# Kernel optimization log

Hardware: AMD Instinct MI355X
Metric: run time of the kernel (lower is better)

The kernel has to match this reference:

```python
import jax, jax.numpy as jnp
import numpy as np


def gcn_conv(x, src, dst, W, b, n_nodes):
    # PyG GCNConv with self-loops and symmetric normalization.
    h = x @ W                                        # [N, out]
    deg = jax.ops.segment_sum(jnp.ones_like(dst, dtype=h.dtype), dst,
                              num_segments=n_nodes)  # includes self-loops
    dinv = jnp.where(deg > 0, jax.lax.rsqrt(deg), 0.0)
    norm = dinv[src] * dinv[dst]                     # [E]
    msg = h[src] * norm[:, None]                     # gather + scale
    out = jax.ops.segment_sum(msg, dst, num_segments=n_nodes)
    return out + b


def setup_inputs() -> dict:
    key = jax.random.key(0)
    ks = jax.random.split(key, 16)
    N, E, F_IN, H, H2, C = 150000, 2400000, 61, 32, 16, 3
    x = jax.random.normal(ks[0], (N, F_IN), dtype=jnp.float32)
    edge_index = jax.random.randint(ks[1], (2, E), 0, N, dtype=jnp.int64)

    def lin(k, fin, fout):
        kw, kb = jax.random.split(k)
        s = 1.0 / np.sqrt(fin)
        W = jax.random.uniform(kw, (fin, fout), jnp.float32, -s, s)
        b = jax.random.uniform(kb, (fout,), jnp.float32, -s, s)
        return W, b

    W1, b1 = lin(ks[2], F_IN, H)
    W2, b2 = lin(ks[3], H, H)
    W3, b3 = lin(ks[4], H, H)
    W4, b4 = lin(ks[5], H, H)
    Wl1, bl1 = lin(ks[6], H, H2)
    Wl2, bl2 = lin(ks[7], H2, C)
    return {"x": x, "edge_index": edge_index,
            "W1": W1, "b1": b1, "W2": W2, "b2": b2,
            "W3": W3, "b3": b3, "W4": W4, "b4": b4,
            "Wl1": Wl1, "bl1": bl1, "Wl2": Wl2, "bl2": bl2}


def reference(x, edge_index, W1, b1, W2, b2, W3, b3, W4, b4, Wl1, bl1, Wl2, bl2):
    n = x.shape[0]
    loops = jnp.arange(n, dtype=edge_index.dtype)
    src = jnp.concatenate([edge_index[0], loops])
    dst = jnp.concatenate([edge_index[1], loops])
    # dropout p=0.25 is identity in eval mode
    h = jax.nn.relu(gcn_conv(x, src, dst, W1, b1, n))
    h = jax.nn.relu(gcn_conv(h, src, dst, W2, b2, n))
    h = jax.nn.relu(gcn_conv(h, src, dst, W3, b3, n))
    h = jax.nn.relu(gcn_conv(h, src, dst, W4, b4, n))
    g = jnp.sum(h, axis=0)                           # sum pool over all nodes -> [32]
    g = jax.nn.relu(g @ Wl1 + bl1)
    return g @ Wl2 + bl2                             # [3]
```

## Files before the change

### kernel.cpp

```cpp
#include <hip/hip_runtime.h>
#include <hip/hip_fp16.h>

#define F_IN 61
#define H 32
#define BUCK_BITS 8
#define BUCK_SZ   256
#define CHUNK     8192
#define XPAD 72

typedef _Float16 f16x8 __attribute__((ext_vector_type(8)));
typedef float    f32x4 __attribute__((ext_vector_type(4)));

__global__ __launch_bounds__(256) void scan1_kernel(const int* __restrict__ in,
                                                    int* __restrict__ scanned,
                                                    int* __restrict__ btot, int n) {
    __shared__ int s[256];
    int tid = threadIdx.x;
    int i = blockIdx.x * 256 + tid;
    int v = (i < n) ? in[i] : 0;
    s[tid] = v;
    __syncthreads();
    for (int off = 1; off < 256; off <<= 1) {
        int t = (tid >= off) ? s[tid - off] : 0;
        __syncthreads();
        s[tid] += t;
        __syncthreads();
    }
    if (i < n) scanned[i] = s[tid] - v;
    if (tid == 255) btot[blockIdx.x] = s[255];
}

__global__ __launch_bounds__(1024) void scan2_kernel(int* __restrict__ btot, int nB) {
    __shared__ int s[1024];
    int tid = threadIdx.x;
    int v = (tid < nB) ? btot[tid] : 0;
    s[tid] = v;
    __syncthreads();
    for (int off = 1; off < 1024; off <<= 1) {
        int t = (tid >= off) ? s[tid - off] : 0;
        __syncthreads();
        s[tid] += t;
        __syncthreads();
    }
    if (tid < nB) btot[tid] = s[tid] - v;
}

__global__ __launch_bounds__(256) void histA_kernel(const int* __restrict__ ei,
                                                    int* __restrict__ counts,
                                                    float* __restrict__ gs,
                                                    int E, int B, int nbuck) {
    __shared__ int h[640];
    int tid = threadIdx.x;
    if (blockIdx.x == 0) {
        #pragma unroll
        for (int r = 0; r < 8; r++) gs[r * 256 + tid] = 0.f;
    }
    for (int i = tid; i < nbuck; i += 256) h[i] = 0;
    __syncthreads();
    int e0 = blockIdx.x * CHUNK;
    int e1 = e0 + CHUNK; if (e1 > E) e1 = E;
    for (int e = e0 + tid; e < e1; e += 256)
        atomicAdd(&h[ei[E + e] >> BUCK_BITS], 1);
    __syncthreads();
    for (int i = tid; i < nbuck; i += 256) counts[i * B + blockIdx.x] = h[i];
}

__global__ __launch_bounds__(256) void binB_kernel(const int* __restrict__ ei,
                                                   const int* __restrict__ countsS,
                                                   const int* __restrict__ btot,
                                                   int* __restrict__ tmp,
                                                   int E, int B, int nbuck) {
    __shared__ int lcur[640];
    int tid = threadIdx.x;
    for (int i = tid; i < nbuck; i += 256) {
        int ci = i * B + blockIdx.x;
        lcur[i] = countsS[ci] + btot[ci >> 8];
    }
    __syncthreads();
    int e0 = blockIdx.x * CHUNK;
    int e1 = e0 + CHUNK; if (e1 > E) e1 = E;
    for (int e = e0 + tid; e < e1; e += 256) {
        int s = ei[e];
        int d = ei[E + e];
        int pos = atomicAdd(&lcur[d >> BUCK_BITS], 1);
        tmp[pos] = (s << BUCK_BITS) | (d & (BUCK_SZ - 1));
    }
}

__global__ __launch_bounds__(256) void binC_kernel(const int* __restrict__ countsS,
                                                   const int* __restrict__ btot,
                                                   const int* __restrict__ tmp,
                                                   int* __restrict__ src_sorted,
                                                   int* __restrict__ row_start,
                                                   float* __restrict__ dinv,
                                                   __half* __restrict__ bufA,
                                                   __half* __restrict__ bufB,
                                                   int N, int E, int B, int nbuck) {
    __shared__ int hist[BUCK_SZ];
    __shared__ int pre[BUCK_SZ];
    __shared__ int lcur[BUCK_SZ];
    int tid = threadIdx.x;
    int b = blockIdx.x;
    int base = b << BUCK_BITS;
    if (b == 0 && tid < H) {
        bufA[(size_t)N * H + tid] = __float2half(0.f);
        bufB[(size_t)N * H + tid] = __float2half(0.f);
    }
    int c0 = b * B;
    int e0 = countsS[c0] + btot[c0 >> 8];
    int e1 = E;
    if (b + 1 < nbuck) {
        int c1 = (b + 1) * B;
        e1 = countsS[c1] + btot[c1 >> 8];
    }
    hist[tid] = 0;
    __syncthreads();
    for (int e = e0 + tid; e < e1; e += 256)
        atomicAdd(&hist[tmp[e] & (BUCK_SZ - 1)], 1);
    __syncthreads();
    int v = hist[tid];
    pre[tid] = v;
    __syncthreads();
    for (int off = 1; off < 256; off <<= 1) {
        int t = (tid >= off) ? pre[tid - off] : 0;
        __syncthreads();
        pre[tid] += t;
        __syncthreads();
    }
    int excl = pre[tid] - v;
    int node = base + tid;
    if (node < N) {
        row_start[node] = e0 + excl;
        dinv[node] = rsqrtf((float)v + 1.0f);
        if (node == N - 1) row_start[N] = E;
    }
    lcur[tid] = e0 + excl;
    __syncthreads();
    for (int e = e0 + tid; e < e1; e += 256) {
        int p = tmp[e];
        int pos = atomicAdd(&lcur[p & (BUCK_SZ - 1)], 1);
        src_sorted[pos] = (p >> BUCK_BITS) << 6;
    }
}

__global__ __launch_bounds__(256) void gemm1_kernel(const float* __restrict__ x,
                                                    const float* __restrict__ W,
                                                    const float* __restrict__ dinv,
                                                    __half* __restrict__ h, int N) {
    __shared__ _Float16 Wt[H * XPAD];
    __shared__ _Float16 xs[64 * XPAD];
    int tid = threadIdx.x;
    for (int i = tid; i < 2048; i += 256) {
        int k = i >> 5, f = i & 31;
        Wt[f * XPAD + k] = (k < F_IN) ? (_Float16)W[k * H + f] : (_Float16)0.f;
    }
    int nb = blockIdx.x * 64;
    int navail = N - nb; if (navail > 64) navail = 64;
    int lim = navail * F_IN;
    const float* xb = x + (long long)nb * F_IN;
    for (int i = tid; i < 64 * F_IN; i += 256) {
        int n = i / F_IN, k = i - n * F_IN;
        xs[n * XPAD + k] = (i < lim) ? (_Float16)xb[i] : (_Float16)0.f;
    }
    if (tid < 192) {
        int n = tid / 3, k = F_IN + (tid - n * 3);
        xs[n * XPAD + k] = (_Float16)0.f;
    }
    __syncthreads();
    int w = tid >> 6, lane = tid & 63;
    int l16 = lane & 15, g = lane >> 4;
    const f16x8* ax  = (const f16x8*)&xs[(w * 16 + l16) * XPAD + g * 8];
    const f16x8* bw0 = (const f16x8*)&Wt[l16 * XPAD + g * 8];
    const f16x8* bw1 = (const f16x8*)&Wt[(16 + l16) * XPAD + g * 8];
    f16x8 a0 = ax[0],  a1 = ax[4];
    f16x8 b00 = bw0[0], b01 = bw0[4];
    f16x8 b10 = bw1[0], b11 = bw1[4];
    f32x4 acc0 = {0.f, 0.f, 0.f, 0.f};
    f32x4 acc1 = {0.f, 0.f, 0.f, 0.f};
    acc0 = __builtin_amdgcn_mfma_f32_16x16x32_f16(a0, b00, acc0, 0, 0, 0);
    acc0 = __builtin_amdgcn_mfma_f32_16x16x32_f16(a1, b01, acc0, 0, 0, 0);
    acc1 = __builtin_amdgcn_mfma_f32_16x16x32_f16(a0, b10, acc1, 0, 0, 0);
    acc1 = __builtin_amdgcn_mfma_f32_16x16x32_f16(a1, b11, acc1, 0, 0, 0);
    int nodebase = nb + w * 16 + g * 4;
    #pragma unroll
    for (int r = 0; r < 4; r++) {
        int node = nodebase + r;
        if (node < N) {
            float di = dinv[node];
            h[(long long)node * H + l16]      = __float2half(acc0[r] * di);
            h[(long long)node * H + 16 + l16] = __float2half(acc1[r] * di);
        }
    }
}

__global__ __launch_bounds__(256) void agg_gemm_kernel(const int* __restrict__ row_start,
                                                       const int* __restrict__ src_sorted,
                                                       const float* __restrict__ dinv,
                                                       const __half* __restrict__ hs,
                                                       const float* __restrict__ b,
                                                       const float* __restrict__ Wn,
                                                       __half* __restrict__ hout, int N) {
    __shared__ float Ws[H * H];
    __shared__ float t[8 * H];
    int tid = threadIdx.x;
    for (int i = tid; i < H * H; i += 256) Ws[i] = Wn[i];
    int nl = tid >> 5;
    int lane32 = tid & 31;
    int p = lane32 >> 4;
    int fp = lane32 & 15;
    int node = blockIdx.x * 8 + nl;
    int zoff = N << 6;
    __half2 accA = __floats2half2_rn(0.f, 0.f);
    __half2 accB = __floats2half2_rn(0.f, 0.f);
    if (node < N) {
        const char* hbase = (const char*)hs + (fp << 2);
        int e0 = row_start[node], e1 = row_start[node + 1];
        int idxv = (e0 + lane32 < e1) ? src_sorted[e0 + lane32] : zoff;
        for (int base = e0; base < e1; base += 32) {
            int w = e1 - base; if (w > 32) w = 32;
            int idxN = (base + 32 + lane32 < e1) ? src_sorted[base + 32 + lane32] : zoff;
            for (int j = 0; j < w; j += 16) {
                int offs[8];
                #pragma unroll
                for (int k = 0; k < 8; k++) offs[k] = __shfl(idxv, j + 2 * k + p, 32);
                unsigned g[8];
                #pragma unroll
                for (int k = 0; k < 8; k++) g[k] = *(const unsigned*)(hbase + offs[k]);
                #pragma unroll
                for (int k = 0; k < 8; k += 2) {
                    accA = __hadd2(accA, *(__half2*)&g[k]);
                    accB = __hadd2(accB, *(__half2*)&g[k + 1]);
                }
            }
            idxv = idxN;
        }
    }
    __half2 accH = __hadd2(accA, accB);
    float2 acc = __half22float2(accH);
    acc.x += __shfl_xor(acc.x, 16, 32);
    acc.y += __shfl_xor(acc.y, 16, 32);
    if (node < N && p == 0) {
        float di = dinv[node];
        unsigned sv = *(const unsigned*)((const char*)hs + ((long long)node << 6) + (fp << 2));
        float2 s2 = __half22float2(*(__half2*)&sv);
        float2 bv = ((const float2*)b)[fp];
        float rx = fmaxf(di * (acc.x + s2.x) + bv.x, 0.f);
        float ry = fmaxf(di * (acc.y + s2.y) + bv.y, 0.f);
        ((float2*)&t[nl * H])[fp] = make_float2(rx, ry);
    }
    __syncthreads();
    if (node < N) {
        int f = lane32;
        float s = 0.f;
        #pragma unroll
        for (int k = 0; k < H; k++) s += t[nl * H + k] * Ws[k * H + f];
        hout[(long long)node * H + f] = __float2half(s * dinv[node]);
    }
}

__global__ __launch_bounds__(256) void agg_pool_kernel(const int* __restrict__ row_start,
                                                       const int* __restrict__ src_sorted,
                                                       const float* __restrict__ dinv,
                                                       const __half* __restrict__ hs,
                                                       const float* __restrict__ b,
                                                       float* __restrict__ gs, int N) {
    __shared__ float t[8 * H];
    int tid = threadIdx.x;
    int nl = tid >> 5;
    int lane32 = tid & 31;
    int p = lane32 >> 4;
    int fp = lane32 & 15;
    int node = blockIdx.x * 8 + nl;
    int zoff = N << 6;
    __half2 accA = __floats2half2_rn(0.f, 0.f);
    __half2 accB = __floats2half2_rn(0.f, 0.f);
    if (node < N) {
        const char* hbase = (const char*)hs + (fp << 2);
        int e0 = row_start[node], e1 = row_start[node + 1];
        int idxv = (e0 + lane32 < e1) ? src_sorted[e0 + lane32] : zoff;
        for (int base = e0; base < e1; base += 32) {
            int w = e1 - base; if (w > 32) w = 32;
            int idxN = (base + 32 + lane32 < e1) ? src_sorted[base + 32 + lane32] : zoff;
            for (int j = 0; j < w; j += 16) {
                int offs[8];
                #pragma unroll
                for (int k = 0; k < 8; k++) offs[k] = __shfl(idxv, j + 2 * k + p, 32);
                unsigned g[8];
                #pragma unroll
                for (int k = 0; k < 8; k++) g[k] = *(const unsigned*)(hbase + offs[k]);
                #pragma unroll
                for (int k = 0; k < 8; k += 2) {
                    accA = __hadd2(accA, *(__half2*)&g[k]);
                    accB = __hadd2(accB, *(__half2*)&g[k + 1]);
                }
            }
            idxv = idxN;
        }
    }
    __half2 accH = __hadd2(accA, accB);
    float2 acc = __half22float2(accH);
    acc.x += __shfl_xor(acc.x, 16, 32);
    acc.y += __shfl_xor(acc.y, 16, 32);
    if (p == 0) {
        float2 r = make_float2(0.f, 0.f);
        if (node < N) {
            float di = dinv[node];
            unsigned sv = *(const unsigned*)((const char*)hs + ((long long)node << 6) + (fp << 2));
            float2 s2 = __half22float2(*(__half2*)&sv);
            float2 bv = ((const float2*)b)[fp];
            r.x = fmaxf(di * (acc.x + s2.x) + bv.x, 0.f);
            r.y = fmaxf(di * (acc.y + s2.y) + bv.y, 0.f);
        }
        ((float2*)&t[nl * H])[fp] = r;
    }
    __syncthreads();
    if (tid < H) {
        float s = 0.f;
        #pragma unroll
        for (int rI = 0; rI < 8; rI++) s += t[rI * H + tid];
        atomicAdd(&gs[(blockIdx.x & 63) * H + tid], s);
    }
}

__global__ __launch_bounds__(64) void head_kernel(const float* __restrict__ gs,
                                                  const float* __restrict__ Wl1,
                                                  const float* __restrict__ bl1,
                                                  const float* __restrict__ Wl2,
                                                  const float* __restrict__ bl2,
                                                  float* __restrict__ out) {
    __shared__ float gg[H];
    __shared__ float t[16];
    int tid = threadIdx.x;
    if (tid < H) {
        float s = 0.f;
        for (int c = 0; c < 64; c++) s += gs[c * H + tid];
        gg[tid] = s;
    }
    __syncthreads();
    if (tid < 16) {
        float s = bl1[tid];
        #pragma unroll
        for (int k = 0; k < 32; k++) s += gg[k] * Wl1[k * 16 + tid];
        t[tid] = fmaxf(s, 0.f);
    }
    __syncthreads();
    if (tid < 3) {
        float s = bl2[tid];
        #pragma unroll
        for (int k = 0; k < 16; k++) s += t[k] * Wl2[k * 3 + tid];
        out[tid] = s;
    }
}

extern "C" void kernel_launch(void* const* d_in, const int* in_sizes, int n_in,
                              void* d_out, int out_size, void* d_ws, size_t ws_size,
                              hipStream_t stream) {
    const float* x   = (const float*)d_in[0];
    const int*   ei  = (const int*)d_in[1];
    const float* W1  = (const float*)d_in[2];
    const float* b1  = (const float*)d_in[3];
    const float* W2  = (const float*)d_in[4];
    const float* b2  = (const float*)d_in[5];
    const float* W3  = (const float*)d_in[6];
    const float* b3  = (const float*)d_in[7];
    const float* W4  = (const float*)d_in[8];
    const float* b4  = (const float*)d_in[9];
    const float* Wl1 = (const float*)d_in[10];
    const float* bl1 = (const float*)d_in[11];
    const float* Wl2 = (const float*)d_in[12];
    const float* bl2 = (const float*)d_in[13];
    float* out = (float*)d_out;

    const int N = in_sizes[0] / F_IN;
    const int E = in_sizes[1] / 2;
    const int nbuck = (N + BUCK_SZ - 1) >> BUCK_BITS;
    const int B = (E + CHUNK - 1) / CHUNK;
    const int nC = nbuck * B;

    char* ws = (char*)d_ws;
    size_t off = 0;
    auto alloc = [&](size_t bytes) {
        char* p = ws + off;
        off += (bytes + 255) & ~(size_t)255;
        return p;
    };
    float* dinv       = (float*)alloc((size_t)N * 4);
    int*   row_start  = (int*)alloc((size_t)(N + 1) * 4);
    int*   counts     = (int*)alloc((size_t)nC * 4);
    int*   countsS    = (int*)alloc((size_t)nC * 4);
    int*   btot2      = (int*)alloc(((size_t)nC / 256 + 2) * 4);
    int*   src_sorted = (int*)alloc((size_t)E * 4);
    int*   tmp        = (int*)alloc((size_t)E * 4);
    __half* bufA      = (__half*)alloc((size_t)(N + 1) * H * 2);
    __half* bufB      = (__half*)alloc((size_t)(N + 1) * H * 2);
    float* gs         = (float*)alloc(64 * H * 4);

    const int TB = 256;
    const int gC  = (nC + TB - 1) / TB;
    const int gN8 = (N + 7) / 8;
    const int gN64 = (N + 63) / 64;

    histA_kernel<<<B, TB, 0, stream>>>(ei, counts, gs, E, B, nbuck);
    scan1_kernel<<<gC, TB, 0, stream>>>(counts, countsS, btot2, nC);
    scan2_kernel<<<1, 1024, 0, stream>>>(btot2, gC);
    binB_kernel<<<B, TB, 0, stream>>>(ei, countsS, btot2, tmp, E, B, nbuck);
    binC_kernel<<<nbuck, TB, 0, stream>>>(countsS, btot2, tmp, src_sorted, row_start,
                                          dinv, bufA, bufB, N, E, B, nbuck);

    gemm1_kernel<<<gN64, TB, 0, stream>>>(x, W1, dinv, bufA, N);
    agg_gemm_kernel<<<gN8, TB, 0, stream>>>(row_start, src_sorted, dinv, bufA, b1, W2, bufB, N);
    agg_gemm_kernel<<<gN8, TB, 0, stream>>>(row_start, src_sorted, dinv, bufB, b2, W3, bufA, N);
    agg_gemm_kernel<<<gN8, TB, 0, stream>>>(row_start, src_sorted, dinv, bufA, b3, W4, bufB, N);
    agg_pool_kernel<<<gN8, TB, 0, stream>>>(row_start, src_sorted, dinv, bufB, b4, gs, N);

    head_kernel<<<1, 64, 0, stream>>>(gs, Wl1, bl1, Wl2, bl2, out);
}
```

Baseline: 361.2 us.

## Stage bucket edges in LDS for binning and use nontemporal index loads and stores

The bin kernel now caches each bucket's edges in shared memory when they fit, and scatters the sorted sources into an LDS output buffer before writing them out coalesced. This avoids rereading tmp from global memory and avoids scattered global writes. Separately, the aggregation kernels read src_sorted with nontemporal loads and write hout with nontemporal stores, so the streaming index traffic leaves cache room for the gathered features. The 48KB of extra LDS per block may lower occupancy in binC, and the nontemporal hout store could hurt if the next layer rereads it from cache.

```diff
diff --git a/kernel.cpp b/kernel.cpp
--- a/kernel.cpp
+++ b/kernel.cpp
@@ -7,6 +7,7 @@
 #define BUCK_SZ   256
 #define CHUNK     8192
 #define XPAD 72
+#define CMAX 6144
 
 typedef _Float16 f16x8 __attribute__((ext_vector_type(8)));
 typedef float    f32x4 __attribute__((ext_vector_type(4)));
@@ -99,6 +100,8 @@
     __shared__ int hist[BUCK_SZ];
     __shared__ int pre[BUCK_SZ];
     __shared__ int lcur[BUCK_SZ];
+    __shared__ int ebuf[CMAX];
+    __shared__ int obuf[CMAX];
     int tid = threadIdx.x;
     int b = blockIdx.x;
     int base = b << BUCK_BITS;
@@ -113,10 +116,20 @@
         int c1 = (b + 1) * B;
         e1 = countsS[c1] + btot[c1 >> 8];
     }
+    int cnt = e1 - e0;
+    bool fits = (cnt <= CMAX);
     hist[tid] = 0;
     __syncthreads();
-    for (int e = e0 + tid; e < e1; e += 256)
-        atomicAdd(&hist[tmp[e] & (BUCK_SZ - 1)], 1);
+    if (fits) {
+        for (int j = tid; j < cnt; j += 256) {
+            int p = tmp[e0 + j];
+            ebuf[j] = p;
+            atomicAdd(&hist[p & (BUCK_SZ - 1)], 1);
+        }
+    } else {
+        for (int j = tid; j < cnt; j += 256)
+            atomicAdd(&hist[tmp[e0 + j] & (BUCK_SZ - 1)], 1);
+    }
     __syncthreads();
     int v = hist[tid];
     pre[tid] = v;
@@ -134,12 +147,23 @@
         dinv[node] = rsqrtf((float)v + 1.0f);
         if (node == N - 1) row_start[N] = E;
     }
-    lcur[tid] = e0 + excl;
-    __syncthreads();
-    for (int e = e0 + tid; e < e1; e += 256) {
-        int p = tmp[e];
-        int pos = atomicAdd(&lcur[p & (BUCK_SZ - 1)], 1);
-        src_sorted[pos] = (p >> BUCK_BITS) << 6;
+    lcur[tid] = fits ? excl : (e0 + excl);
+    __syncthreads();
+    if (fits) {
+        for (int j = tid; j < cnt; j += 256) {
+            int p = ebuf[j];
+            int pos = atomicAdd(&lcur[p & (BUCK_SZ - 1)], 1);
+            obuf[pos] = (p >> BUCK_BITS) << 6;
+        }
+        __syncthreads();
+        for (int j = tid; j < cnt; j += 256)
+            src_sorted[e0 + j] = obuf[j];
+    } else {
+        for (int j = tid; j < cnt; j += 256) {
+            int p = tmp[e0 + j];
+            int pos = atomicAdd(&lcur[p & (BUCK_SZ - 1)], 1);
+            src_sorted[pos] = (p >> BUCK_BITS) << 6;
+        }
     }
 }
 
@@ -215,10 +239,12 @@
     if (node < N) {
         const char* hbase = (const char*)hs + (fp << 2);
         int e0 = row_start[node], e1 = row_start[node + 1];
-        int idxv = (e0 + lane32 < e1) ? src_sorted[e0 + lane32] : zoff;
+        int idxv = zoff;
+        if (e0 + lane32 < e1) idxv = __builtin_nontemporal_load(src_sorted + e0 + lane32);
         for (int base = e0; base < e1; base += 32) {
             int w = e1 - base; if (w > 32) w = 32;
-            int idxN = (base + 32 + lane32 < e1) ? src_sorted[base + 32 + lane32] : zoff;
+            int idxN = zoff;
+            if (base + 32 + lane32 < e1) idxN = __builtin_nontemporal_load(src_sorted + base + 32 + lane32);
             for (int j = 0; j < w; j += 16) {
                 int offs[8];
                 #pragma unroll
@@ -254,7 +280,9 @@
         float s = 0.f;
         #pragma unroll
         for (int k = 0; k < H; k++) s += t[nl * H + k] * Ws[k * H + f];
-        hout[(long long)node * H + f] = __float2half(s * dinv[node]);
+        __half hv = __float2half(s * dinv[node]);
+        __builtin_nontemporal_store(__half_as_ushort(hv),
+                                    (unsigned short*)&hout[(long long)node * H + f]);
     }
 }
 
@@ -277,10 +305,12 @@
     if (node < N) {
         const char* hbase = (const char*)hs + (fp << 2);
         int e0 = row_start[node], e1 = row_start[node + 1];
-        int idxv = (e0 + lane32 < e1) ? src_sorted[e0 + lane32] : zoff;
+        int idxv = zoff;
+        if (e0 + lane32 < e1) idxv = __builtin_nontemporal_load(src_sorted + e0 + lane32);
         for (int base = e0; base < e1; base += 32) {
             int w = e1 - base; if (w > 32) w = 32;
-            int idxN = (base + 32 + lane32 < e1) ? src_sorted[base + 32 + lane32] : zoff;
+            int idxN = zoff;
+            if (base + 32 + lane32 < e1) idxN = __builtin_nontemporal_load(src_sorted + base + 32 + lane32);
             for (int j = 0; j < w; j += 16) {
                 int offs[8];
                 #pragma unroll
```

Result: no change. 363.5 us (+0.6%).

## Replace two-level bucketed CSR build with global-atomic degree count and scatter

Applied to the files above, without the earlier changes.

Replaces the bucketed counting sort (per-chunk bucket histograms, scan, binning into a temp array, per-bucket local sort) with a simpler CSR build: global atomic degree count per node, a scan over N nodes, then a scatter of edges into place using global atomic cursors. This drops the tmp array and one full pass over the edges, and the scan kernel now handles four elements per thread so it covers more than 1024 blocks. In exchange it relies on random global atomics on 150K counters, which may contend or be slower than LDS atomics, and the order of edges within each row is no longer deterministic.

```diff
diff --git a/kernel.cpp b/kernel.cpp
--- a/kernel.cpp
+++ b/kernel.cpp
@@ -3,9 +3,6 @@
 
 #define F_IN 61
 #define H 32
-#define BUCK_BITS 8
-#define BUCK_SZ   256
-#define CHUNK     8192
 #define XPAD 72
 
 typedef _Float16 f16x8 __attribute__((ext_vector_type(8)));
@@ -33,8 +30,13 @@
 __global__ __launch_bounds__(1024) void scan2_kernel(int* __restrict__ btot, int nB) {
     __shared__ int s[1024];
     int tid = threadIdx.x;
-    int v = (tid < nB) ? btot[tid] : 0;
-    s[tid] = v;
+    int base = tid << 2;
+    int v0 = (base + 0 < nB) ? btot[base + 0] : 0;
+    int v1 = (base + 1 < nB) ? btot[base + 1] : 0;
+    int v2 = (base + 2 < nB) ? btot[base + 2] : 0;
+    int v3 = (base + 3 < nB) ? btot[base + 3] : 0;
+    int sum = v0 + v1 + v2 + v3;
+    s[tid] = sum;
     __syncthreads();
     for (int off = 1; off < 1024; off <<= 1) {
         int t = (tid >= off) ? s[tid - off] : 0;
@@ -42,104 +44,59 @@
         s[tid] += t;
         __syncthreads();
     }
-    if (tid < nB) btot[tid] = s[tid] - v;
-}
-
-__global__ __launch_bounds__(256) void histA_kernel(const int* __restrict__ ei,
-                                                    int* __restrict__ counts,
-                                                    float* __restrict__ gs,
-                                                    int E, int B, int nbuck) {
-    __shared__ int h[640];
+    int run = s[tid] - sum;
+    if (base + 0 < nB) { btot[base + 0] = run; run += v0; }
+    if (base + 1 < nB) { btot[base + 1] = run; run += v1; }
+    if (base + 2 < nB) { btot[base + 2] = run; run += v2; }
+    if (base + 3 < nB) { btot[base + 3] = run; }
+}
+
+__global__ __launch_bounds__(256) void deg_kernel(const int* __restrict__ ei,
+                                                  int* __restrict__ deg,
+                                                  float* __restrict__ gs,
+                                                  __half* __restrict__ bufA,
+                                                  __half* __restrict__ bufB,
+                                                  int E, int N) {
     int tid = threadIdx.x;
     if (blockIdx.x == 0) {
         #pragma unroll
         for (int r = 0; r < 8; r++) gs[r * 256 + tid] = 0.f;
-    }
-    for (int i = tid; i < nbuck; i += 256) h[i] = 0;
-    __syncthreads();
-    int e0 = blockIdx.x * CHUNK;
-    int e1 = e0 + CHUNK; if (e1 > E) e1 = E;
-    for (int e = e0 + tid; e < e1; e += 256)
-        atomicAdd(&h[ei[E + e] >> BUCK_BITS], 1);
-    __syncthreads();
-    for (int i = tid; i < nbuck; i += 256) counts[i * B + blockIdx.x] = h[i];
-}
-
-__global__ __launch_bounds__(256) void binB_kernel(const int* __restrict__ ei,
-                                                   const int* __restrict__ countsS,
-                                                   const int* __restrict__ btot,
-                                                   int* __restrict__ tmp,
-                                                   int E, int B, int nbuck) {
-    __shared__ int lcur[640];
-    int tid = threadIdx.x;
-    for (int i = tid; i < nbuck; i += 256) {
-        int ci = i * B + blockIdx.x;
-        lcur[i] = countsS[ci] + btot[ci >> 8];
-    }
-    __syncthreads();
-    int e0 = blockIdx.x * CHUNK;
-    int e1 = e0 + CHUNK; if (e1 > E) e1 = E;
-    for (int e = e0 + tid; e < e1; e += 256) {
-        int s = ei[e];
+        if (tid < H) {
+            bufA[(size_t)N * H + tid] = __float2half(0.f);
+            bufB[(size_t)N * H + tid] = __float2half(0.f);
+        }
+    }
+    int stride = gridDim.x * 256;
+    for (int e = blockIdx.x * 256 + tid; e < E; e += stride)
+        atomicAdd(&deg[ei[E + e]], 1);
+}
+
+__global__ __launch_bounds__(256) void finalize_kernel(const int* __restrict__ scanned,
+                                                       const int* __restrict__ btot,
+                                                       const int* __restrict__ deg,
+                                                       int* __restrict__ row_start,
+                                                       int* __restrict__ cur,
+                                                       float* __restrict__ dinv,
+                                                       int N, int E) {
+    int node = blockIdx.x * 256 + threadIdx.x;
+    if (node < N) {
+        int rs = scanned[node] + btot[node >> 8];
+        row_start[node] = rs;
+        cur[node] = rs;
+        dinv[node] = rsqrtf((float)deg[node] + 1.0f);
+        if (node == N - 1) row_start[N] = E;
+    }
+}
+
+__global__ __launch_bounds__(256) void scatter_kernel(const int* __restrict__ ei,
+                                                      int* __restrict__ cur,
+                                                      int* __restrict__ src_sorted,
+                                                      int E) {
+    int stride = gridDim.x * 256;
+    for (int e = blockIdx.x * 256 + threadIdx.x; e < E; e += stride) {
         int d = ei[E + e];
-        int pos = atomicAdd(&lcur[d >> BUCK_BITS], 1);
-        tmp[pos] = (s << BUCK_BITS) | (d & (BUCK_SZ - 1));
-    }
-}
-
-__global__ __launch_bounds__(256) void binC_kernel(const int* __restrict__ countsS,
-                                                   const int* __restrict__ btot,
-                                                   const int* __restrict__ tmp,
-                                                   int* __restrict__ src_sorted,
-                                                   int* __restrict__ row_start,
-                                                   float* __restrict__ dinv,
-                                                   __half* __restrict__ bufA,
-                                                   __half* __restrict__ bufB,
-                                                   int N, int E, int B, int nbuck) {
-    __shared__ int hist[BUCK_SZ];
-    __shared__ int pre[BUCK_SZ];
-    __shared__ int lcur[BUCK_SZ];
-    int tid = threadIdx.x;
-    int b = blockIdx.x;
-    int base = b << BUCK_BITS;
-    if (b == 0 && tid < H) {
-        bufA[(size_t)N * H + tid] = __float2half(0.f);
-        bufB[(size_t)N * H + tid] = __float2half(0.f);
-    }
-    int c0 = b * B;
-    int e0 = countsS[c0] + btot[c0 >> 8];
-    int e1 = E;
-    if (b + 1 < nbuck) {
-        int c1 = (b + 1) * B;
-        e1 = countsS[c1] + btot[c1 >> 8];
-    }
-    hist[tid] = 0;
-    __syncthreads();
-    for (int e = e0 + tid; e < e1; e += 256)
-        atomicAdd(&hist[tmp[e] & (BUCK_SZ - 1)], 1);
-    __syncthreads();
-    int v = hist[tid];
-    pre[tid] = v;
-    __syncthreads();
-    for (int off = 1; off < 256; off <<= 1) {
-        int t = (tid >= off) ? pre[tid - off] : 0;
-        __syncthreads();
-        pre[tid] += t;
-        __syncthreads();
-    }
-    int excl = pre[tid] - v;
-    int node = base + tid;
-    if (node < N) {
-        row_start[node] = e0 + excl;
-        dinv[node] = rsqrtf((float)v + 1.0f);
-        if (node == N - 1) row_start[N] = E;
-    }
-    lcur[tid] = e0 + excl;
-    __syncthreads();
-    for (int e = e0 + tid; e < e1; e += 256) {
-        int p = tmp[e];
-        int pos = atomicAdd(&lcur[p & (BUCK_SZ - 1)], 1);
-        src_sorted[pos] = (p >> BUCK_BITS) << 6;
+        int pos = atomicAdd(&cur[d], 1);
+        src_sorted[pos] = ei[e] << 6;
     }
 }
 
@@ -373,9 +330,6 @@
 
     const int N = in_sizes[0] / F_IN;
     const int E = in_sizes[1] / 2;
-    const int nbuck = (N + BUCK_SZ - 1) >> BUCK_BITS;
-    const int B = (E + CHUNK - 1) / CHUNK;
-    const int nC = nbuck * B;
 
     char* ws = (char*)d_ws;
     size_t off = 0;
@@ -386,26 +340,27 @@
     };
     float* dinv       = (float*)alloc((size_t)N * 4);
     int*   row_start  = (int*)alloc((size_t)(N + 1) * 4);
-    int*   counts     = (int*)alloc((size_t)nC * 4);
-    int*   countsS    = (int*)alloc((size_t)nC * 4);
-    int*   btot2      = (int*)alloc(((size_t)nC / 256 + 2) * 4);
+    int*   deg        = (int*)alloc((size_t)N * 4);
+    int*   scanned    = (int*)alloc((size_t)N * 4);
+    int*   btotN      = (int*)alloc(((size_t)N / 256 + 2) * 4);
+    int*   cur        = (int*)alloc((size_t)N * 4);
     int*   src_sorted = (int*)alloc((size_t)E * 4);
-    int*   tmp        = (int*)alloc((size_t)E * 4);
     __half* bufA      = (__half*)alloc((size_t)(N + 1) * H * 2);
     __half* bufB      = (__half*)alloc((size_t)(N + 1) * H * 2);
     float* gs         = (float*)alloc(64 * H * 4);
 
     const int TB = 256;
-    const int gC  = (nC + TB - 1) / TB;
-    const int gN8 = (N + 7) / 8;
+    const int gN   = (N + TB - 1) / TB;
+    const int gN8  = (N + 7) / 8;
     const int gN64 = (N + 63) / 64;
-
-    histA_kernel<<<B, TB, 0, stream>>>(ei, counts, gs, E, B, nbuck);
-    scan1_kernel<<<gC, TB, 0, stream>>>(counts, countsS, btot2, nC);
-    scan2_kernel<<<1, 1024, 0, stream>>>(btot2, gC);
-    binB_kernel<<<B, TB, 0, stream>>>(ei, countsS, btot2, tmp, E, B, nbuck);
-    binC_kernel<<<nbuck, TB, 0, stream>>>(countsS, btot2, tmp, src_sorted, row_start,
-                                          dinv, bufA, bufB, N, E, B, nbuck);
+    const int gE   = 2048;
+
+    hipMemsetAsync(deg, 0, (size_t)N * 4, stream);
+    deg_kernel<<<gE, TB, 0, stream>>>(ei, deg, gs, bufA, bufB, E, N);
+    scan1_kernel<<<gN, TB, 0, stream>>>(deg, scanned, btotN, N);
+    scan2_kernel<<<1, 1024, 0, stream>>>(btotN, gN);
+    finalize_kernel<<<gN, TB, 0, stream>>>(scanned, btotN, deg, row_start, cur, dinv, N, E);
+    scatter_kernel<<<gE, TB, 0, stream>>>(ei, cur, src_sorted, E);
 
     gemm1_kernel<<<gN64, TB, 0, stream>>>(x, W1, dinv, bufA, N);
     agg_gemm_kernel<<<gN8, TB, 0, stream>>>(row_start, src_sorted, dinv, bufA, b1, W2, bufB, N);
```

Result: slower. 598.8 us (+65.8%).
